# Kernel tuning notes

Measured on AMD Instinct MI355X. Metric: run time of the kernel, lower is better.

## Reference

```python
import jax, jax.numpy as jnp
import numpy as np
from jax import lax

B, C, L, G = 2048, 9605, 20, 50
ALPHA, ALPHA1, ALPHA2, ALPHA3, ALPHA_OTHER = 0.5, 0.05, 2.0, 10.0, 0.5
NEG_INF = jnp.float32(-1e30)


def setup_inputs() -> dict:
    k0, k1, k2, k3 = jax.random.split(jax.random.key(0), 4)
    x = jax.random.normal(k0, (B, C), jnp.float32)
    # sparse multi-label targets (~10 positives/row) so at most ~1 whitelist group is active,
    # matching the original code's assert len(gt_whitelist_index) == 1
    y = (jax.random.uniform(k1, (B, C)) < 0.001).astype(jnp.int32)
    y_neg = (jax.random.uniform(k2, (B, C)) < 0.001).astype(jnp.int32)
    # L disjoint whitelist groups of G classes each (from mapping_dict in the original)
    idx = jax.random.permutation(k3, C)[: L * G].reshape(L, G)
    group_mask = jnp.zeros((L, C), bool).at[jnp.arange(L)[:, None], idx].set(True)
    return {"x": x, "y": y, "y_neg": y_neg, "group_mask": group_mask}


def _rank_loss(x1, x2, margin):
    # our_rank_loss: sigmoid(alpha3*(x2-x1+margin)), scaled by alpha2 when positive
    d = x2 - x1 + margin
    s = jax.nn.sigmoid(ALPHA3 * d)
    return jnp.where(d > 0, ALPHA2 * s, s)


def reference(x, y, y_neg, group_mask):
    xs = jax.nn.sigmoid(x)  # [B, C]
    gmf = group_mask.astype(jnp.float32)  # [L, C]

    # per-row max score inside each whitelist group -> [B, L]
    # lax.map over the L (=20) groups keeps peak memory at one [B, C] temp per step
    group_max = lax.map(
        lambda m: jnp.max(jnp.where(m, xs, NEG_INF), axis=-1), group_mask
    ).T  # [B, L]

    # find_gt_whitelist: group k active iff sum(y[group_k]) > 0
    active = jnp.einsum("bc,lc->bl", y.astype(jnp.float32), gmf) > 0
    active_neg = jnp.einsum("bc,lc->bl", y_neg.astype(jnp.float32), gmf) > 0
    has_gt = jnp.any(active, axis=-1)  # [B]
    g = jnp.argmax(active, axis=-1)  # first active group (original asserts exactly one)

    # top_k_thres = max(11th largest sigmoid score, alpha_other) in both branches
    thres = jnp.maximum(lax.top_k(xs, 11)[0][:, 10], ALPHA_OTHER)  # [B]

    # max over union of all whitelist classes (wl_indices)
    union_max = jnp.max(jnp.where(jnp.any(group_mask, 0)[None, :], xs, NEG_INF), -1)

    gt_max = jnp.take_along_axis(group_max, g[:, None], axis=1)[:, 0]  # [B]
    # incorrect_max: max(0, max over groups != g); incorrect_neg: max(0, max over neg-active groups)
    excl = jnp.where(jnp.arange(L)[None, :] == g[:, None], NEG_INF, group_max)
    incorrect_max = jnp.maximum(jnp.max(excl, -1), 0.0)
    incorrect_neg = jnp.maximum(jnp.max(jnp.where(active_neg, group_max, 0.0), -1), 0.0)

    # branch A: no gt whitelist group active
    case_a = (1 - ALPHA) * _rank_loss(thres, union_max, ALPHA1) + ALPHA * _rank_loss(
        thres, incorrect_neg, ALPHA1
    )
    # branch B: exactly one gt group g
    case_b = (
        _rank_loss(gt_max, thres, ALPHA1)
        + jnp.where(
            incorrect_max > 0, (1 - ALPHA) * _rank_loss(thres, incorrect_max, ALPHA1), 0.0
        )
        + jnp.where(
            incorrect_neg > 0,
            ALPHA * _rank_loss(thres, incorrect_neg, ALPHA1),
            ALPHA * _rank_loss(thres, incorrect_max, ALPHA1),
        )
    )
    return jnp.sum(jnp.where(has_gt, case_b, case_a))
```

## Files before the change

kernel.cpp:

```cpp
#include <hip/hip_runtime.h>
#include <stdint.h>

#define B_ROWS 2048
#define C_CLS  9605
#define L_GRP  20
#define GM_BYTES (L_GRP * C_CLS)
#define REPSTRIDE 9728
#define GID_REGION (4 * REPSTRIDE)
#define PARTIAL_OFF (64 + GID_REGION)
#define NEG_BIG -3.0e38f

__device__ __forceinline__ float sigmoidf(float v) {
  return 1.0f / (1.0f + __expf(-v));
}

__device__ __forceinline__ float rank_loss(float x1, float x2) {
  float d = x2 - x1 + 0.05f;
  float s = 1.0f / (1.0f + __expf(-10.0f * d));
  return d > 0.0f ? 2.0f * s : s;
}

__device__ __forceinline__ unsigned fmap(float f) {
  unsigned u = __float_as_uint(f);
  return (u & 0x80000000u) ? ~u : (u | 0x80000000u);
}
__device__ __forceinline__ float funmap(unsigned m) {
  unsigned u = (m & 0x80000000u) ? (m ^ 0x80000000u) : ~m;
  return __uint_as_float(u);
}

__global__ void probe_init_kernel(const uint4* __restrict__ gm,
                                  unsigned char* __restrict__ ws,
                                  float* __restrict__ out,
                                  int* __restrict__ flag) {
  __shared__ int s_part[16];
  const int tid = threadIdx.x;
  if (tid == 0) out[0] = 0.0f;
  uint4* gfill = (uint4*)(ws + 64);
  const unsigned F = 0xFFFFFFFFu;
  for (int i = tid; i < GID_REGION / 16; i += 1024)
    gfill[i] = make_uint4(F, F, F, F);
  int local = 0;
  const int nvec = GM_BYTES / 16;
  for (int i = tid; i < nvec; i += 1024) {
    uint4 w = gm[i];
    unsigned a[4] = {w.x, w.y, w.z, w.w};
#pragma unroll
    for (int q = 0; q < 4; ++q) {
      local += ((a[q] & 0x000000FFu) != 0) + ((a[q] & 0x0000FF00u) != 0) +
               ((a[q] & 0x00FF0000u) != 0) + ((a[q] & 0xFF000000u) != 0);
    }
  }
  if (tid == 0) {
    const unsigned char* gb = (const unsigned char*)gm;
    for (int i = nvec * 16; i < GM_BYTES; ++i) local += (gb[i] != 0);
  }
#pragma unroll
  for (int off = 32; off; off >>= 1) local += __shfl_xor(local, off);
  if ((tid & 63) == 0) s_part[tid >> 6] = local;
  __syncthreads();
  if (tid == 0) {
    int tot = 0;
    for (int w = 0; w < 16; ++w) tot += s_part[w];
    *flag = tot;
  }
}

__global__ void build_gid_kernel(const void* gm, const int* __restrict__ flag,
                                 unsigned char* __restrict__ ws) {
  int i = blockIdx.x * blockDim.x + threadIdx.x;
  if (i >= GM_BYTES) return;
  const bool is_byte = (*flag > 600);
  bool m;
  if (is_byte) m = ((const unsigned char*)gm)[i] != 0;
  else         m = ((const unsigned int*)gm)[i] != 0u;
  if (m) {
    int l = i / C_CLS;
    int c = i - l * C_CLS;
    unsigned char* base = ws + 64;
#pragma unroll
    for (int r = 0; r < 4; ++r) base[r * REPSTRIDE + r + c] = (unsigned char)l;
  }
}

__global__ __launch_bounds__(256, 4) void loss_kernel(
    const float* __restrict__ x, const int* __restrict__ y,
    const int* __restrict__ yn, const unsigned char* __restrict__ ws64,
    float* __restrict__ partial) {
  __shared__ unsigned s_gmax[L_GRP];
  __shared__ unsigned s_act, s_actn;
  __shared__ float s_wtop[4 * 11];
  const int tid = threadIdx.x;
  const int lane = tid & 63;
  const int wave = tid >> 6;
  const int row = blockIdx.x;

  const size_t base = (size_t)row * C_CLS;
  const int mis = (int)(base & 3);
  const int peel = (4 - mis) & 3;
  const float* xr = x + base;
  const int* yr = y + base;
  const int* nr = yn + base;
  const unsigned char* gidc = ws64 + mis * REPSTRIDE + mis;

  if (tid < L_GRP) s_gmax[tid] = 0u;
  if (tid == 0) { s_act = 0u; s_actn = 0u; }
  __syncthreads();

  float t[11];
#pragma unroll
  for (int i = 0; i < 11; ++i) t[i] = 0.0f;
  unsigned actL = 0u, actnL = 0u;

  auto ins = [&](float v) {
    if (v > t[10]) {
      float a = v;
#pragma unroll
      for (int i = 0; i < 11; ++i) {
        float hi = fmaxf(t[i], a); a = fminf(t[i], a); t[i] = hi;
      }
    }
  };
  auto gmax_upd = [&](unsigned gk, float v) {
    unsigned fm = fmap(v);
    if (fm > s_gmax[gk]) atomicMax(&s_gmax[gk], fm);
  };
  auto edge = [&](int c) {
    float v = xr[c];
    ins(v);
    unsigned gk = gidc[c];
    if (gk < L_GRP) {
      gmax_upd(gk, v);
      unsigned bit = 1u << gk;
      if (yr[c] != 0) actL |= bit;
      if (nr[c] != 0) actnL |= bit;
    }
  };

  if (tid < peel) edge(tid);
  const int nvec = (C_CLS - peel) >> 2;
  const int tail0 = peel + (nvec << 2);
  if (tid < C_CLS - tail0) edge(tail0 + tid);

  const float4* x4 = (const float4*)(xr + peel);
  const int4* y4 = (const int4*)(yr + peel);
  const int4* n4 = (const int4*)(nr + peel);
  const unsigned* g4 = (const unsigned*)(gidc + peel);

  for (int j = tid; j < nvec; j += 256) {
    float4 xv = x4[j];
    int4 yv = y4[j];
    int4 nv = n4[j];
    unsigned gw = g4[j];

    if (gw != 0xFFFFFFFFu) {
      unsigned g0 = gw & 0xFFu, g1 = (gw >> 8) & 0xFFu,
               g2 = (gw >> 16) & 0xFFu, g3 = gw >> 24;
      if (g0 < L_GRP) gmax_upd(g0, xv.x);
      if (g1 < L_GRP) gmax_upd(g1, xv.y);
      if (g2 < L_GRP) gmax_upd(g2, xv.z);
      if (g3 < L_GRP) gmax_upd(g3, xv.w);
    }
    if (yv.x | yv.y | yv.z | yv.w | nv.x | nv.y | nv.z | nv.w) {
      const int yq[4] = {yv.x, yv.y, yv.z, yv.w};
      const int nq[4] = {nv.x, nv.y, nv.z, nv.w};
      const unsigned gq[4] = {gw & 0xFFu, (gw >> 8) & 0xFFu,
                              (gw >> 16) & 0xFFu, gw >> 24};
#pragma unroll
      for (int q = 0; q < 4; ++q) {
        if ((yq[q] | nq[q]) && gq[q] < L_GRP) {
          unsigned bit = 1u << gq[q];
          if (yq[q]) actL |= bit;
          if (nq[q]) actnL |= bit;
        }
      }
    }
    float am = fmaxf(fmaxf(xv.x, xv.y), fmaxf(xv.z, xv.w));
    if (am > t[10]) { ins(xv.x); ins(xv.y); ins(xv.z); ins(xv.w); }
  }

  if (actL) atomicOr(&s_act, actL);
  if (actnL) atomicOr(&s_actn, actnL);

  float cur = t[0];
  float mr[11];
#pragma unroll
  for (int r = 0; r < 11; ++r) {
    float m = cur;
#pragma unroll
    for (int off = 32; off; off >>= 1) m = fmaxf(m, __shfl_xor(m, off));
    mr[r] = m;
    if (r < 10) {
      unsigned long long b = __ballot(cur == m);
      int leader = (int)(__ffsll(b) - 1);
      if (lane == leader) {
#pragma unroll
        for (int i = 0; i < 10; ++i) t[i] = t[i + 1];
        t[10] = NEG_BIG;
        cur = t[0];
      }
    }
  }
  if (lane == 0) {
#pragma unroll
    for (int r = 0; r < 11; ++r) s_wtop[wave * 11 + r] = mr[r];
  }
  __syncthreads();

  if (wave == 0) {
    float v = (lane < 44) ? s_wtop[lane] : NEG_BIG;
    float eleventh = NEG_BIG;
#pragma unroll
    for (int r = 0; r < 11; ++r) {
      float m = v;
#pragma unroll
      for (int off = 32; off; off >>= 1) m = fmaxf(m, __shfl_xor(m, off));
      eleventh = m;
      if (r < 10) {
        unsigned long long b = __ballot(v == m);
        int leader = (int)(__ffsll(b) - 1);
        if (lane == leader) v = NEG_BIG;
      }
    }

    const unsigned aL = s_act, anL = s_actn;
    const bool has_gt = (aL != 0u);
    const int g = has_gt ? (__ffs(aL) - 1) : 0;
    const float thres = fmaxf(sigmoidf(eleventh), 0.5f);

    float union_max = NEG_BIG, gt_sg = 0.0f, inc_max = NEG_BIG, inc_neg = 0.0f;
#pragma unroll
    for (int l = 0; l < L_GRP; ++l) {
      float sg = sigmoidf(funmap(s_gmax[l]));
      union_max = fmaxf(union_max, sg);
      if (l == g) gt_sg = sg; else inc_max = fmaxf(inc_max, sg);
      if ((anL >> l) & 1u) inc_neg = fmaxf(inc_neg, sg);
    }
    inc_max = fmaxf(inc_max, 0.0f);
    inc_neg = fmaxf(inc_neg, 0.0f);

    float loss;
    if (has_gt) {
      loss = rank_loss(gt_sg, thres);
      if (inc_max > 0.0f) loss += 0.5f * rank_loss(thres, inc_max);
      loss += 0.5f * rank_loss(thres, (inc_neg > 0.0f) ? inc_neg : inc_max);
    } else {
      loss = 0.5f * rank_loss(thres, union_max) + 0.5f * rank_loss(thres, inc_neg);
    }
    if (lane == 0) partial[row] = loss;
  }
}

__global__ void reduce_kernel(const float* __restrict__ partial,
                              float* __restrict__ out) {
  __shared__ float s_p[4];
  const int tid = threadIdx.x;
  float v = 0.0f;
#pragma unroll
  for (int k = 0; k < B_ROWS / 256; ++k) v += partial[tid + k * 256];
#pragma unroll
  for (int off = 32; off; off >>= 1) v += __shfl_xor(v, off);
  if ((tid & 63) == 0) s_p[tid >> 6] = v;
  __syncthreads();
  if (tid == 0) out[0] = s_p[0] + s_p[1] + s_p[2] + s_p[3];
}

extern "C" void kernel_launch(void* const* d_in, const int* in_sizes, int n_in,
                              void* d_out, int out_size, void* d_ws, size_t ws_size,
                              hipStream_t stream) {
  (void)in_sizes; (void)n_in; (void)out_size; (void)ws_size;
  const float* x = (const float*)d_in[0];
  const int* y = (const int*)d_in[1];
  const int* yn = (const int*)d_in[2];
  const void* gm = d_in[3];

  int* flag = (int*)d_ws;
  unsigned char* ws = (unsigned char*)d_ws;
  unsigned char* ws64 = ws + 64;
  float* partial = (float*)(ws + PARTIAL_OFF);

  probe_init_kernel<<<1, 1024, 0, stream>>>((const uint4*)gm, ws,
                                            (float*)d_out, flag);
  build_gid_kernel<<<(GM_BYTES + 255) / 256, 256, 0, stream>>>(gm, flag, ws);
  loss_kernel<<<B_ROWS, 256, 0, stream>>>(x, y, yn, ws64, partial);
  reduce_kernel<<<1, 256, 0, stream>>>(partial, (float*)d_out);
}
```

Before: 256.2 us.

## Batch four strided vector loads per iteration and fold final reduction into atomics

The main streaming loop now issues 16 loads (x, y, y_neg and group ids for four strided positions) before processing any of them. This raises memory-level parallelism for the bandwidth-bound row scan. The separate reduce kernel is removed, and each row block atomically adds its loss into the output, which saves a launch. In exchange, register pressure rises under the 256x4 launch bounds, and the float atomics make the summation order nondeterministic. The output is assumed to be zeroed by the init kernel.

```diff
diff --git a/kernel.cpp b/kernel.cpp
--- a/kernel.cpp
+++ b/kernel.cpp
@@ -7,7 +7,6 @@
 #define GM_BYTES (L_GRP * C_CLS)
 #define REPSTRIDE 9728
 #define GID_REGION (4 * REPSTRIDE)
-#define PARTIAL_OFF (64 + GID_REGION)
 #define NEG_BIG -3.0e38f
 
 __device__ __forceinline__ float sigmoidf(float v) {
@@ -86,7 +85,7 @@
 __global__ __launch_bounds__(256, 4) void loss_kernel(
     const float* __restrict__ x, const int* __restrict__ y,
     const int* __restrict__ yn, const unsigned char* __restrict__ ws64,
-    float* __restrict__ partial) {
+    float* __restrict__ out) {
   __shared__ unsigned s_gmax[L_GRP];
   __shared__ unsigned s_act, s_actn;
   __shared__ float s_wtop[4 * 11];
@@ -147,12 +146,7 @@
   const int4* n4 = (const int4*)(nr + peel);
   const unsigned* g4 = (const unsigned*)(gidc + peel);
 
-  for (int j = tid; j < nvec; j += 256) {
-    float4 xv = x4[j];
-    int4 yv = y4[j];
-    int4 nv = n4[j];
-    unsigned gw = g4[j];
-
+  auto quad = [&](float4 xv, int4 yv, int4 nv, unsigned gw) {
     if (gw != 0xFFFFFFFFu) {
       unsigned g0 = gw & 0xFFu, g1 = (gw >> 8) & 0xFFu,
                g2 = (gw >> 16) & 0xFFu, g3 = gw >> 24;
@@ -177,6 +171,33 @@
     }
     float am = fmaxf(fmaxf(xv.x, xv.y), fmaxf(xv.z, xv.w));
     if (am > t[10]) { ins(xv.x); ins(xv.y); ins(xv.z); ins(xv.w); }
+  };
+
+  int j = tid;
+  for (; j + 768 < nvec; j += 1024) {
+    float4 xa = x4[j];
+    float4 xb = x4[j + 256];
+    float4 xc = x4[j + 512];
+    float4 xd = x4[j + 768];
+    int4 ya = y4[j];
+    int4 yb = y4[j + 256];
+    int4 yc = y4[j + 512];
+    int4 yd = y4[j + 768];
+    int4 na = n4[j];
+    int4 nb = n4[j + 256];
+    int4 nc = n4[j + 512];
+    int4 nd = n4[j + 768];
+    unsigned ga = g4[j];
+    unsigned gb = g4[j + 256];
+    unsigned gc = g4[j + 512];
+    unsigned gd = g4[j + 768];
+    quad(xa, ya, na, ga);
+    quad(xb, yb, nb, gb);
+    quad(xc, yc, nc, gc);
+    quad(xd, yd, nd, gd);
+  }
+  for (; j < nvec; j += 256) {
+    quad(x4[j], y4[j], n4[j], g4[j]);
   }
 
   if (actL) atomicOr(&s_act, actL);
@@ -247,22 +268,8 @@
     } else {
       loss = 0.5f * rank_loss(thres, union_max) + 0.5f * rank_loss(thres, inc_neg);
     }
-    if (lane == 0) partial[row] = loss;
-  }
-}
-
-__global__ void reduce_kernel(const float* __restrict__ partial,
-                              float* __restrict__ out) {
-  __shared__ float s_p[4];
-  const int tid = threadIdx.x;
-  float v = 0.0f;
-#pragma unroll
-  for (int k = 0; k < B_ROWS / 256; ++k) v += partial[tid + k * 256];
-#pragma unroll
-  for (int off = 32; off; off >>= 1) v += __shfl_xor(v, off);
-  if ((tid & 63) == 0) s_p[tid >> 6] = v;
-  __syncthreads();
-  if (tid == 0) out[0] = s_p[0] + s_p[1] + s_p[2] + s_p[3];
+    if (lane == 0) atomicAdd(out, loss);
+  }
 }
 
 extern "C" void kernel_launch(void* const* d_in, const int* in_sizes, int n_in,
@@ -277,11 +284,9 @@
   int* flag = (int*)d_ws;
   unsigned char* ws = (unsigned char*)d_ws;
   unsigned char* ws64 = ws + 64;
-  float* partial = (float*)(ws + PARTIAL_OFF);
 
   probe_init_kernel<<<1, 1024, 0, stream>>>((const uint4*)gm, ws,
                                             (float*)d_out, flag);
   build_gid_kernel<<<(GM_BYTES + 255) / 256, 256, 0, stream>>>(gm, flag, ws);
-  loss_kernel<<<B_ROWS, 256, 0, stream>>>(x, y, yn, ws64, partial);
-  reduce_kernel<<<1, 256, 0, stream>>>(partial, (float*)d_out);
-}
+  loss_kernel<<<B_ROWS, 256, 0, stream>>>(x, y, yn, ws64, (float*)d_out);
+}
```

Measured after the change: 255.1 us. About the same (-0.5%).

## Parallelize mask probe, use nontemporal loads, fold final reduction into atomics

Applied to the files above, without the earlier changes.

The single-block mask probe/fill kernel becomes a 256-block grid that writes per-block counts, which the gid builder reduces in every block. The separate reduce kernel is dropped, and each row's loss is atomically added into the output. The main streaming loads of x, y and y_neg become nontemporal. This removes one launch and a serial 1024-thread pass, at the cost of atomic contention on a single float and a nondeterministic summation order.

```diff
diff --git a/kernel.cpp b/kernel.cpp
--- a/kernel.cpp
+++ b/kernel.cpp
@@ -7,8 +7,11 @@
 #define GM_BYTES (L_GRP * C_CLS)
 #define REPSTRIDE 9728
 #define GID_REGION (4 * REPSTRIDE)
-#define PARTIAL_OFF (64 + GID_REGION)
+#define PCOUNT_OFF (64 + GID_REGION)
 #define NEG_BIG -3.0e38f
+
+typedef float f32x4 __attribute__((ext_vector_type(4)));
+typedef unsigned u32x4 __attribute__((ext_vector_type(4)));
 
 __device__ __forceinline__ float sigmoidf(float v) {
   return 1.0f / (1.0f + __expf(-v));
@@ -29,48 +32,58 @@
   return __uint_as_float(u);
 }
 
-__global__ void probe_init_kernel(const uint4* __restrict__ gm,
-                                  unsigned char* __restrict__ ws,
-                                  float* __restrict__ out,
-                                  int* __restrict__ flag) {
-  __shared__ int s_part[16];
+__global__ __launch_bounds__(256) void probe_init_kernel(
+    const uint4* __restrict__ gm, unsigned char* __restrict__ ws,
+    float* __restrict__ out, int* __restrict__ pcount) {
+  __shared__ int s_part[4];
   const int tid = threadIdx.x;
-  if (tid == 0) out[0] = 0.0f;
+  const int bid = blockIdx.x;
+  const int gtid = bid * 256 + tid;
+
+  if (gtid == 0) out[0] = 0.0f;
   uint4* gfill = (uint4*)(ws + 64);
   const unsigned F = 0xFFFFFFFFu;
-  for (int i = tid; i < GID_REGION / 16; i += 1024)
-    gfill[i] = make_uint4(F, F, F, F);
+  if (gtid < GID_REGION / 16) gfill[gtid] = make_uint4(F, F, F, F);
+
   int local = 0;
   const int nvec = GM_BYTES / 16;
-  for (int i = tid; i < nvec; i += 1024) {
-    uint4 w = gm[i];
+  if (gtid < nvec) {
+    uint4 w = gm[gtid];
     unsigned a[4] = {w.x, w.y, w.z, w.w};
 #pragma unroll
     for (int q = 0; q < 4; ++q) {
       local += ((a[q] & 0x000000FFu) != 0) + ((a[q] & 0x0000FF00u) != 0) +
                ((a[q] & 0x00FF0000u) != 0) + ((a[q] & 0xFF000000u) != 0);
     }
-  }
-  if (tid == 0) {
-    const unsigned char* gb = (const unsigned char*)gm;
-    for (int i = nvec * 16; i < GM_BYTES; ++i) local += (gb[i] != 0);
+  } else if (gtid == nvec) {
+    unsigned a = ((const unsigned*)gm)[nvec * 4];
+    local += ((a & 0x000000FFu) != 0) + ((a & 0x0000FF00u) != 0) +
+             ((a & 0x00FF0000u) != 0) + ((a & 0xFF000000u) != 0);
   }
 #pragma unroll
   for (int off = 32; off; off >>= 1) local += __shfl_xor(local, off);
   if ((tid & 63) == 0) s_part[tid >> 6] = local;
   __syncthreads();
-  if (tid == 0) {
-    int tot = 0;
-    for (int w = 0; w < 16; ++w) tot += s_part[w];
-    *flag = tot;
-  }
-}
-
-__global__ void build_gid_kernel(const void* gm, const int* __restrict__ flag,
-                                 unsigned char* __restrict__ ws) {
-  int i = blockIdx.x * blockDim.x + threadIdx.x;
+  if (tid == 0) pcount[bid] = s_part[0] + s_part[1] + s_part[2] + s_part[3];
+}
+
+__global__ __launch_bounds__(256) void build_gid_kernel(
+    const void* gm, const int* __restrict__ pcount,
+    unsigned char* __restrict__ ws) {
+  __shared__ int s_part[4];
+  __shared__ int s_total;
+  const int tid = threadIdx.x;
+  int v = pcount[tid];
+#pragma unroll
+  for (int off = 32; off; off >>= 1) v += __shfl_xor(v, off);
+  if ((tid & 63) == 0) s_part[tid >> 6] = v;
+  __syncthreads();
+  if (tid == 0) s_total = s_part[0] + s_part[1] + s_part[2] + s_part[3];
+  __syncthreads();
+  const bool is_byte = (s_total > 600);
+
+  const int i = blockIdx.x * 256 + tid;
   if (i >= GM_BYTES) return;
-  const bool is_byte = (*flag > 600);
   bool m;
   if (is_byte) m = ((const unsigned char*)gm)[i] != 0;
   else         m = ((const unsigned int*)gm)[i] != 0u;
@@ -86,7 +99,7 @@
 __global__ __launch_bounds__(256, 4) void loss_kernel(
     const float* __restrict__ x, const int* __restrict__ y,
     const int* __restrict__ yn, const unsigned char* __restrict__ ws64,
-    float* __restrict__ partial) {
+    float* __restrict__ out) {
   __shared__ unsigned s_gmax[L_GRP];
   __shared__ unsigned s_act, s_actn;
   __shared__ float s_wtop[4 * 11];
@@ -142,15 +155,15 @@
   const int tail0 = peel + (nvec << 2);
   if (tid < C_CLS - tail0) edge(tail0 + tid);
 
-  const float4* x4 = (const float4*)(xr + peel);
-  const int4* y4 = (const int4*)(yr + peel);
-  const int4* n4 = (const int4*)(nr + peel);
+  const f32x4* x4 = (const f32x4*)(xr + peel);
+  const u32x4* y4 = (const u32x4*)(yr + peel);
+  const u32x4* n4 = (const u32x4*)(nr + peel);
   const unsigned* g4 = (const unsigned*)(gidc + peel);
 
   for (int j = tid; j < nvec; j += 256) {
-    float4 xv = x4[j];
-    int4 yv = y4[j];
-    int4 nv = n4[j];
+    f32x4 xv = __builtin_nontemporal_load(x4 + j);
+    u32x4 yv = __builtin_nontemporal_load(y4 + j);
+    u32x4 nv = __builtin_nontemporal_load(n4 + j);
     unsigned gw = g4[j];
 
     if (gw != 0xFFFFFFFFu) {
@@ -162,8 +175,8 @@
       if (g3 < L_GRP) gmax_upd(g3, xv.w);
     }
     if (yv.x | yv.y | yv.z | yv.w | nv.x | nv.y | nv.z | nv.w) {
-      const int yq[4] = {yv.x, yv.y, yv.z, yv.w};
-      const int nq[4] = {nv.x, nv.y, nv.z, nv.w};
+      const unsigned yq[4] = {yv.x, yv.y, yv.z, yv.w};
+      const unsigned nq[4] = {nv.x, nv.y, nv.z, nv.w};
       const unsigned gq[4] = {gw & 0xFFu, (gw >> 8) & 0xFFu,
                               (gw >> 16) & 0xFFu, gw >> 24};
 #pragma unroll
@@ -247,22 +260,8 @@
     } else {
       loss = 0.5f * rank_loss(thres, union_max) + 0.5f * rank_loss(thres, inc_neg);
     }
-    if (lane == 0) partial[row] = loss;
-  }
-}
-
-__global__ void reduce_kernel(const float* __restrict__ partial,
-                              float* __restrict__ out) {
-  __shared__ float s_p[4];
-  const int tid = threadIdx.x;
-  float v = 0.0f;
-#pragma unroll
-  for (int k = 0; k < B_ROWS / 256; ++k) v += partial[tid + k * 256];
-#pragma unroll
-  for (int off = 32; off; off >>= 1) v += __shfl_xor(v, off);
-  if ((tid & 63) == 0) s_p[tid >> 6] = v;
-  __syncthreads();
-  if (tid == 0) out[0] = s_p[0] + s_p[1] + s_p[2] + s_p[3];
+    if (lane == 0) atomicAdd(out, loss);
+  }
 }
 
 extern "C" void kernel_launch(void* const* d_in, const int* in_sizes, int n_in,
@@ -274,14 +273,12 @@
   const int* yn = (const int*)d_in[2];
   const void* gm = d_in[3];
 
-  int* flag = (int*)d_ws;
   unsigned char* ws = (unsigned char*)d_ws;
   unsigned char* ws64 = ws + 64;
-  float* partial = (float*)(ws + PARTIAL_OFF);
-
-  probe_init_kernel<<<1, 1024, 0, stream>>>((const uint4*)gm, ws,
-                                            (float*)d_out, flag);
-  build_gid_kernel<<<(GM_BYTES + 255) / 256, 256, 0, stream>>>(gm, flag, ws);
-  loss_kernel<<<B_ROWS, 256, 0, stream>>>(x, y, yn, ws64, partial);
-  reduce_kernel<<<1, 256, 0, stream>>>(partial, (float*)d_out);
-}
+  int* pcount = (int*)(ws + PCOUNT_OFF);
+
+  probe_init_kernel<<<256, 256, 0, stream>>>((const uint4*)gm, ws,
+                                             (float*)d_out, pcount);
+  build_gid_kernel<<<(GM_BYTES + 255) / 256, 256, 0, stream>>>(gm, pcount, ws);
+  loss_kernel<<<B_ROWS, 256, 0, stream>>>(x, y, yn, ws64, (float*)d_out);
+}
```

Measured after the change: 238.6 us. -6.9%, faster.
